# Kernel tuning notes

Hardware: AMD Instinct MI355X
Metric: run time of the kernel (lower is better)

The kernel has to match this reference:

```python
import jax, jax.numpy as jnp
import numpy as np

HEADS, DQK, DV = 4, 128, 128
HH, WW = 32, 32
SCALE = DQK ** -0.5
EPS = 1e-5


def bn(x, g, b, m, v):
    # eval-mode BatchNorm2d over channel dim of NCHW
    inv = g * jax.lax.rsqrt(v + EPS)
    return x * inv[:, None, None] + (b - m * inv)[:, None, None]


def rel_to_abs(x):
    # x: (B, Nh, L, 2L-1) -> (B, Nh, L, L)
    B, Nh, L, _ = x.shape
    x = jnp.pad(x, ((0, 0), (0, 0), (0, 0), (0, 1)))
    fx = x.reshape(B, Nh, L * 2 * L)
    fx = jnp.pad(fx, ((0, 0), (0, 0), (0, L - 1)))
    fx = fx.reshape(B, Nh, L + 1, 2 * L - 1)
    return fx[:, :, :L, L - 1:]


def rel_logits_1d(q, rel_k):
    # q: (B, Nh, H, W, D); rel_k: (2W-1, D)
    B, Nh, H, W, D = q.shape
    r = jnp.einsum('bnhwd,rd->bnhwr', q, rel_k)
    r = rel_to_abs(r.reshape(B, Nh * H, W, 2 * W - 1))
    r = r.reshape(B, Nh, H, W, W)
    return jnp.broadcast_to(r[:, :, :, None], (B, Nh, H, H, W, W))


def pos_bias(q, rel_h, rel_w):
    # q: (B, Nh, H*W, D), already scaled
    B, Nh, L, D = q.shape
    q5 = q.reshape(B, Nh, HH, WW, D)
    rw = rel_logits_1d(q5, rel_w)                     # (B,N,H,Hx,W,W)
    rw = rw.transpose(0, 1, 2, 4, 3, 5).reshape(B, Nh, HH * WW, HH * WW)
    rh = rel_logits_1d(q5.transpose(0, 1, 3, 2, 4), rel_h)  # (B,N,W,Wx,H,H)
    rh = rh.transpose(0, 1, 4, 2, 5, 3).reshape(B, Nh, HH * WW, HH * WW)
    return rw + rh


def to_heads(x):
    # (B, Nh*d, H, W) -> (B, Nh, H*W, d)
    B, C, H, W = x.shape
    x = x.reshape(B, HEADS, C // HEADS, H, W)
    return x.transpose(0, 1, 3, 4, 2).reshape(B, HEADS, H * W, C // HEADS)


def mhsa(x, w_qk, w_v, rel_h, rel_w):
    B, C, H, W = x.shape
    qk = jnp.einsum('bchw,oc->bohw', x, w_qk)
    q, k = jnp.split(qk, 2, axis=1)
    v = jnp.einsum('bchw,oc->bohw', x, w_v)
    q, k, v = to_heads(q), to_heads(k), to_heads(v)
    q = q * SCALE
    logits = jnp.einsum('bnid,bnjd->bnij', q, k) + pos_bias(q, rel_h, rel_w)
    weights = jax.nn.softmax(logits, axis=-1)
    out = jnp.einsum('bnij,bnjd->bnid', weights, v)   # (B,Nh,HW,dv)
    out = out.reshape(B, HEADS, H, W, DV).transpose(0, 1, 4, 2, 3)
    return out.reshape(B, HEADS * DV, H, W)


def setup_inputs() -> dict:
    key = jax.random.key(0)
    ks = jax.random.split(key, 12)
    d = {
        'x': jax.random.normal(ks[0], (8, 512, HH, WW), jnp.float32),
        'w_qk': jax.random.normal(ks[1], (2 * HEADS * DQK, 512), jnp.float32) * 0.02,
        'w_v': jax.random.normal(ks[2], (HEADS * DV, 512), jnp.float32) * 0.02,
        'rel_h': jax.random.normal(ks[3], (2 * HH - 1, DQK), jnp.float32) * SCALE,
        'rel_w': jax.random.normal(ks[4], (2 * WW - 1, DQK), jnp.float32) * SCALE,
        'g1': jnp.ones((512,), jnp.float32),
        'b1': jnp.zeros((512,), jnp.float32),
        'm1': jax.random.normal(ks[5], (512,), jnp.float32) * 0.1,
        'v1': jax.random.uniform(ks[6], (512,), jnp.float32) + 0.5,
        'g2': jnp.ones((512,), jnp.float32),
        'b2': jnp.zeros((512,), jnp.float32),
        'm2': jax.random.normal(ks[7], (512,), jnp.float32) * 0.1,
        'v2': jax.random.uniform(ks[8], (512,), jnp.float32) + 0.5,
        'w_fc': jax.random.normal(ks[9], (512, 512, 3, 3), jnp.float32) * 0.02,
        'bias_fc': jnp.zeros((512,), jnp.float32),
    }
    return d


def reference(x, w_qk, w_v, rel_h, rel_w, g1, b1, m1, v1, g2, b2, m2, v2, w_fc, bias_fc):
    out = jax.nn.relu(bn(x, g1, b1, m1, v1))
    out = mhsa(out, w_qk, w_v, rel_h, rel_w)
    x = out + x
    out = jax.nn.relu(bn(x, g2, b2, m2, v2))
    out = jax.lax.conv_general_dilated(
        out, w_fc, window_strides=(1, 1), padding='SAME',
        dimension_numbers=('NCHW', 'OIHW', 'NCHW')) + bias_fc[:, None, None]
    return out + x
```

## Files before the change

### kernel.cpp

```cpp
#include <hip/hip_runtime.h>

typedef __bf16 v8bf __attribute__((ext_vector_type(8)));
typedef float f32x4 __attribute__((ext_vector_type(4)));

#define DEVI static __device__ __forceinline__

DEVI v8bf load8(const __bf16* p) { return *reinterpret_cast<const v8bf*>(p); }

DEVI f32x4 mfma16(v8bf a, v8bf b, f32x4 c) {
  return __builtin_amdgcn_mfma_f32_16x16x32_bf16(a, b, c, 0, 0, 0);
}

DEVI void gld16(const __bf16* g, __bf16* l) {
  __builtin_amdgcn_global_load_lds(
      (const __attribute__((address_space(1))) unsigned int*)(const void*)g,
      (__attribute__((address_space(3))) unsigned int*)(void*)l, 16, 0, 0);
}

#define SCALE_Q 0.08838834764831845f

__global__ void k_prep(const float* __restrict__ wqk, const float* __restrict__ wv,
                       const float* __restrict__ relh, const float* __restrict__ relw,
                       const float* __restrict__ wfc, __bf16* __restrict__ wqkb,
                       __bf16* __restrict__ wvb, __bf16* __restrict__ rhb,
                       __bf16* __restrict__ rwb, __bf16* __restrict__ Wt,
                       float* __restrict__ zpad4) {
  const int bid = blockIdx.x, tid = threadIdx.x;
  if (bid < 2048) {
    int i = bid * 256 + tid;
    wqkb[i] = (__bf16)wqk[i];
  } else if (bid < 3072) {
    int i = (bid - 2048) * 256 + tid;
    wvb[i] = (__bf16)wv[i];
  } else if (bid < 3104) {
    int i = (bid - 3072) * 256 + tid;
    if (i < 8064) rhb[i] = (__bf16)relh[i];
  } else if (bid < 3136) {
    int i = (bid - 3104) * 256 + tid;
    if (i < 8064) rwb[i] = (__bf16)relw[i];
  } else if (bid < 4160) {
    int i = (bid - 3136) * 256 + tid;
    const float* src = wfc + (size_t)i * 9;
#pragma unroll
    for (int tap = 0; tap < 9; ++tap)
      Wt[(size_t)tap * 262144 + i] = (__bf16)src[tap];
  } else {
    int i = (bid - 4160) * 256 + tid;
    f32x4 z = {0.f, 0.f, 0.f, 0.f};
    reinterpret_cast<f32x4*>(zpad4)[i] = z;
  }
}

__global__ void k_bn1(const float* __restrict__ x, const float* __restrict__ g,
                      const float* __restrict__ bb, const float* __restrict__ m,
                      const float* __restrict__ v, __bf16* __restrict__ y) {
  __shared__ float tile[32][33];
  const int b = blockIdx.z, c0 = blockIdx.y * 32, s0 = blockIdx.x * 32;
  const int tx = threadIdx.x, ty = threadIdx.y;
#pragma unroll
  for (int r = 0; r < 4; ++r) {
    int c = c0 + ty + r * 8;
    float inv = g[c] * rsqrtf(v[c] + 1e-5f);
    float beta = bb[c] - m[c] * inv;
    float val = x[((size_t)b * 512 + c) * 1024 + s0 + tx] * inv + beta;
    tile[ty + r * 8][tx] = fmaxf(val, 0.0f);
  }
  __syncthreads();
#pragma unroll
  for (int r = 0; r < 4; ++r) {
    int s = s0 + ty + r * 8;
    y[((size_t)b * 1024 + s) * 512 + c0 + tx] = (__bf16)tile[tx][ty + r * 8];
  }
}

__global__ void k_bn2(const float* __restrict__ x2, const float* __restrict__ g,
                      const float* __restrict__ bb, const float* __restrict__ m,
                      const float* __restrict__ v, __bf16* __restrict__ zp) {
  __shared__ float tile[32][33];
  const int b = blockIdx.z, c0 = blockIdx.y * 32, s0 = blockIdx.x * 32;
  const int tx = threadIdx.x, ty = threadIdx.y;
#pragma unroll
  for (int r = 0; r < 4; ++r) {
    int c = c0 + ty + r * 8;
    float inv = g[c] * rsqrtf(v[c] + 1e-5f);
    float beta = bb[c] - m[c] * inv;
    float val = x2[((size_t)b * 512 + c) * 1024 + s0 + tx] * inv + beta;
    tile[ty + r * 8][tx] = fmaxf(val, 0.0f);
  }
  __syncthreads();
#pragma unroll
  for (int r = 0; r < 4; ++r) {
    int s = s0 + ty + r * 8;
    int hh = s >> 5, ww = s & 31;
    zp[(((size_t)b * 34 + hh + 1) * 34 + ww + 1) * 512 + c0 + tx] =
        (__bf16)tile[tx][ty + r * 8];
  }
}

__global__ __launch_bounds__(256) void k_proj(
    const __bf16* __restrict__ wall, const __bf16* __restrict__ y,
    __bf16* __restrict__ qout, __bf16* __restrict__ kout,
    __bf16* __restrict__ vout) {
  __shared__ __bf16 As[128 * 32];
  __shared__ __bf16 Bs[128 * 32];
  const int t = threadIdx.x;
  const int wave = t >> 6, lane = t & 63;
  const int l15 = lane & 15, quad = lane >> 4;
  const int mbase = blockIdx.x * 128;
  const int nbase = blockIdx.y * 128;
  const int mh = (wave >> 1) * 64, nh = (wave & 1) * 64;

  const int row0 = t >> 2, part8 = (t & 3) * 8;
  const __bf16* gA0 = wall + (size_t)(mbase + row0) * 512 + part8;
  const __bf16* gA1 = gA0 + (size_t)64 * 512;
  const __bf16* gB0 = y + (size_t)(nbase + row0) * 512 + part8;
  const __bf16* gB1 = gB0 + (size_t)64 * 512;
  __bf16* lA0 = As + (size_t)(wave * 64) * 8;
  __bf16* lA1 = As + (size_t)(256 + wave * 64) * 8;
  __bf16* lB0 = Bs + (size_t)(wave * 64) * 8;
  __bf16* lB1 = Bs + (size_t)(256 + wave * 64) * 8;

  const f32x4 fz = {0.f, 0.f, 0.f, 0.f};
  f32x4 acc[4][4];
#pragma unroll
  for (int i = 0; i < 4; ++i)
#pragma unroll
    for (int j = 0; j < 4; ++j) acc[i][j] = fz;

  for (int k0 = 0; k0 < 512; k0 += 32) {
    __syncthreads();
    gld16(gA0 + k0, lA0);
    gld16(gA1 + k0, lA1);
    gld16(gB0 + k0, lB0);
    gld16(gB1 + k0, lB1);
    __syncthreads();
    v8bf a[4], bfr[4];
#pragma unroll
    for (int i = 0; i < 4; ++i)
      a[i] = load8(&As[(size_t)(mh + i * 16 + l15) * 32 + quad * 8]);
#pragma unroll
    for (int j = 0; j < 4; ++j)
      bfr[j] = load8(&Bs[(size_t)(nh + j * 16 + l15) * 32 + quad * 8]);
#pragma unroll
    for (int i = 0; i < 4; ++i)
#pragma unroll
      for (int j = 0; j < 4; ++j) acc[i][j] = mfma16(a[i], bfr[j], acc[i][j]);
  }

#pragma unroll
  for (int i = 0; i < 4; ++i)
#pragma unroll
    for (int j = 0; j < 4; ++j)
#pragma unroll
      for (int r = 0; r < 4; ++r) {
        int o = mbase + mh + i * 16 + quad * 4 + r;
        int nflat = nbase + nh + j * 16 + l15;
        int b = nflat >> 10, s = nflat & 1023;
        float val = acc[i][j][r];
        if (o < 512) {
          int n = o >> 7, d = o & 127;
          qout[(((size_t)b * 4 + n) * 1024 + s) * 128 + d] = (__bf16)(val * SCALE_Q);
        } else if (o < 1024) {
          int oe = o - 512; int n = oe >> 7, d = oe & 127;
          kout[(((size_t)b * 4 + n) * 1024 + s) * 128 + d] = (__bf16)val;
        } else {
          int oe = o - 1024; int n = oe >> 7, d = oe & 127;
          vout[(((size_t)b * 4 + n) * 128 + d) * 1024 + s] = (__bf16)val;
        }
      }
}

__global__ __launch_bounds__(256, 2) void k_attn(
    const __bf16* __restrict__ q, const __bf16* __restrict__ kmat,
    const __bf16* __restrict__ vt, const __bf16* __restrict__ relh,
    const __bf16* __restrict__ relw, const float* __restrict__ x,
    float* __restrict__ x2) {
  __shared__ __bf16 Ks[4 * 64 * 32];
  __shared__ __bf16 Vs[2 * 128 * 32];
  __shared__ __bf16 P[4 * 16 * 72];
  __shared__ float RWs[64][33];
  __shared__ float RHs[64][33];

  const int Lb = blockIdx.x;
  const int xcd = Lb & 7, local = Lb >> 3;
  const int bn = xcd * 4 + (local & 3);
  const int qblk = local >> 2;
  const int s0 = qblk * 64;

  const int t = threadIdx.x;
  const int wave = t >> 6, lane = t & 63;
  const int l15 = lane & 15, quad = lane >> 4;
  const size_t hoff = ((size_t)bn) << 17;
  const int s0w = s0 + wave * 16;
  const int wlo = (wave & 1) * 16;
  const int h0w = s0w >> 5;

  v8bf aq[4];
  {
    const __bf16* qp = q + hoff + (size_t)(s0w + l15) * 128;
#pragma unroll
    for (int kk = 0; kk < 4; ++kk) aq[kk] = load8(qp + kk * 32 + quad * 8);
  }

#pragma unroll
  for (int nt = 0; nt < 4; ++nt) {
    int rr = nt * 16 + l15;
    const __bf16* bp = relw + (size_t)rr * 128;
    f32x4 acc = {0.f, 0.f, 0.f, 0.f};
#pragma unroll
    for (int kk = 0; kk < 4; ++kk)
      acc = mfma16(aq[kk], load8(bp + kk * 32 + quad * 8), acc);
#pragma unroll
    for (int r = 0; r < 4; ++r) {
      int row = quad * 4 + r;
      int wj = rr + wlo + row - 31;
      if (wj >= 0 && wj < 32) RWs[wave * 16 + row][wj] = acc[r];
    }
  }
#pragma unroll
  for (int nt = 0; nt < 2; ++nt) {
    int hj = nt * 16 + l15;
    const __bf16* bp = relh + (size_t)(hj - h0w + 31) * 128;
    f32x4 acc = {0.f, 0.f, 0.f, 0.f};
#pragma unroll
    for (int kk = 0; kk < 4; ++kk)
      acc = mfma16(aq[kk], load8(bp + kk * 32 + quad * 8), acc);
#pragma unroll
    for (int r = 0; r < 4; ++r) RHs[wave * 16 + quad * 4 + r][hj] = acc[r];
  }

  const int row0 = t >> 2, part8 = (t & 3) * 8;
  const __bf16* kg = kmat + hoff + (size_t)row0 * 128 + part8;
  const __bf16* vg = vt + hoff + (size_t)row0 * 1024 + part8;
  __bf16* ksw = Ks + wave * 512;
  __bf16* vsw = Vs + wave * 512;

  const f32x4 fz = {0.f, 0.f, 0.f, 0.f};
  float lsum[4] = {0.f, 0.f, 0.f, 0.f};
  f32x4 oacc[8];
#pragma unroll
  for (int dt = 0; dt < 8; ++dt) oacc[dt] = fz;
  __bf16* Pw = P + wave * 16 * 72;

#pragma unroll 1
  for (int iter = 0; iter < 16; ++iter) {
    const int j0 = iter * 64;
    __syncthreads();
#pragma unroll
    for (int kk = 0; kk < 4; ++kk)
      gld16(kg + (size_t)j0 * 128 + kk * 32, ksw + kk * 2048);
#pragma unroll
    for (int kk2 = 0; kk2 < 2; ++kk2)
#pragma unroll
      for (int dh = 0; dh < 2; ++dh)
        gld16(vg + (size_t)dh * 64 * 1024 + j0 + kk2 * 32,
              vsw + kk2 * 4096 + dh * 2048);
    __syncthreads();

    f32x4 sacc[4];
#pragma unroll
    for (int nj = 0; nj < 4; ++nj) {
      f32x4 a = fz;
#pragma unroll
      for (int kk = 0; kk < 4; ++kk)
        a = mfma16(aq[kk],
                   load8(&Ks[kk * 2048 + (nj * 16 + l15) * 32 + quad * 8]), a);
      sacc[nj] = a;
    }
#pragma unroll
    for (int nj = 0; nj < 4; ++nj) {
      const int wj = (nj & 1) * 16 + l15;
      const int hj = (j0 + nj * 16) >> 5;
#pragma unroll
      for (int r = 0; r < 4; ++r) {
        const int row = quad * 4 + r;
        const int gi = wave * 16 + row;
        float val = sacc[nj][r] + RWs[gi][wj] + RHs[gi][hj];
        float p = __expf(fminf(val, 60.0f));
        lsum[r] += p;
        Pw[row * 72 + nj * 16 + l15] = (__bf16)p;
      }
    }
    v8bf pf[2];
#pragma unroll
    for (int kk2 = 0; kk2 < 2; ++kk2)
      pf[kk2] = *reinterpret_cast<const v8bf*>(&Pw[l15 * 72 + kk2 * 32 + quad * 8]);
#pragma unroll
    for (int dt = 0; dt < 8; ++dt) {
      f32x4 a = oacc[dt];
#pragma unroll
      for (int kk2 = 0; kk2 < 2; ++kk2)
        a = mfma16(pf[kk2],
                   load8(&Vs[kk2 * 4096 + (dt * 16 + l15) * 32 + quad * 8]), a);
      oacc[dt] = a;
    }
  }

#pragma unroll
  for (int r = 0; r < 4; ++r)
#pragma unroll
    for (int msk = 8; msk >= 1; msk >>= 1) lsum[r] += __shfl_xor(lsum[r], msk);

#pragma unroll
  for (int r = 0; r < 4; ++r) {
    float inv = 1.0f / lsum[r];
    int s = s0w + quad * 4 + r;
#pragma unroll
    for (int dt = 0; dt < 8; ++dt) {
      int d = dt * 16 + l15;
      size_t idx = ((size_t)bn * 128 + d) * 1024 + s;
      x2[idx] = oacc[dt][r] * inv + x[idx];
    }
  }
}

__global__ __launch_bounds__(256, 2) void k_conv(
    const __bf16* __restrict__ Wt, const __bf16* __restrict__ zp,
    float* __restrict__ part) {
  __shared__ __bf16 As[4 * 128 * 32];
  __shared__ __bf16 Bs[4 * 128 * 32];
  const int t = threadIdx.x;
  const int wave = t >> 6, lane = t & 63;
  const int l15 = lane & 15, quad = lane >> 4;

  const int id = blockIdx.x;
  const int combo = id & 7;
  const int ot = combo >> 1, sp = combo & 1;
  const int nt = id >> 3;
  const int mbase = ot * 128;
  const int nbase = nt * 128;
  const int cs = sp * 256;
  const int mh = (wave >> 1) * 64, nh = (wave & 1) * 64;

  const int row0 = t >> 2;
  const int part8 = (t & 3) * 8;
  const __bf16* gA0 = Wt + (size_t)(mbase + row0) * 512 + cs + part8;
  const __bf16* gA1 = gA0 + (size_t)64 * 512;
  const int n0 = nbase + row0;
  const int b0 = n0 >> 10, spn = n0 & 1023;
  const __bf16* gB0 =
      zp + ((size_t)(b0 * 34 + (spn >> 5) + 1) * 34 + (spn & 31) + 1) * 512 + cs + part8;
  const __bf16* gB1 = gB0 + (size_t)2 * 34 * 512;
  const int wofs = wave * 512;

  const f32x4 fz = {0.f, 0.f, 0.f, 0.f};
  f32x4 acc[4][4];
#pragma unroll
  for (int i = 0; i < 4; ++i)
#pragma unroll
    for (int j = 0; j < 4; ++j) acc[i][j] = fz;

#pragma unroll 1
  for (int tap = 0; tap < 9; ++tap) {
    const int dh = tap / 3 - 1, dw = tap % 3 - 1;
    const size_t aoff = (size_t)tap * 512 * 512;
    const int boff = (dh * 34 + dw) * 512;
#pragma unroll 1
    for (int k0 = 0; k0 < 256; k0 += 128) {
      __syncthreads();
#pragma unroll
      for (int c = 0; c < 4; ++c) {
        const int kq = k0 + c * 32;
        gld16(gA0 + aoff + kq, As + c * 4096 + wofs);
        gld16(gA1 + aoff + kq, As + c * 4096 + 2048 + wofs);
        gld16(gB0 + boff + kq, Bs + c * 4096 + wofs);
        gld16(gB1 + boff + kq, Bs + c * 4096 + 2048 + wofs);
      }
      __syncthreads();
#pragma unroll
      for (int c = 0; c < 4; ++c) {
        v8bf a[4], bfr[4];
#pragma unroll
        for (int i = 0; i < 4; ++i)
          a[i] = load8(&As[c * 4096 + (mh + i * 16 + l15) * 32 + quad * 8]);
#pragma unroll
        for (int j = 0; j < 4; ++j)
          bfr[j] = load8(&Bs[c * 4096 + (nh + j * 16 + l15) * 32 + quad * 8]);
#pragma unroll
        for (int i = 0; i < 4; ++i)
#pragma unroll
          for (int j = 0; j < 4; ++j) acc[i][j] = mfma16(a[i], bfr[j], acc[i][j]);
      }
    }
  }

  float* pout = part + (size_t)sp * 8 * 512 * 1024;
#pragma unroll
  for (int i = 0; i < 4; ++i)
#pragma unroll
    for (int j = 0; j < 4; ++j)
#pragma unroll
      for (int r = 0; r < 4; ++r) {
        int o = mbase + mh + i * 16 + quad * 4 + r;
        int nn = nbase + nh + j * 16 + l15;
        int bb2 = nn >> 10, s = nn & 1023;
        pout[((size_t)bb2 * 512 + o) * 1024 + s] = acc[i][j][r];
      }
}

__global__ void k_sum(const float* __restrict__ part, const float* __restrict__ bias,
                      const float* __restrict__ x2, float* __restrict__ out) {
  int i = blockIdx.x * 256 + threadIdx.x;
  int o = (i >> 8) & 511;
  f32x4 p0 = reinterpret_cast<const f32x4*>(part)[i];
  f32x4 p1 = reinterpret_cast<const f32x4*>(part + (size_t)8 * 512 * 1024)[i];
  f32x4 xr = reinterpret_cast<const f32x4*>(x2)[i];
  float bo = bias[o];
  f32x4 r;
#pragma unroll
  for (int c = 0; c < 4; ++c) r[c] = p0[c] + p1[c] + bo + xr[c];
  reinterpret_cast<f32x4*>(out)[i] = r;
}

extern "C" void kernel_launch(void* const* d_in, const int* in_sizes, int n_in,
                              void* d_out, int out_size, void* d_ws, size_t ws_size,
                              hipStream_t stream) {
  const float* x    = (const float*)d_in[0];
  const float* wqk  = (const float*)d_in[1];
  const float* wv   = (const float*)d_in[2];
  const float* relh = (const float*)d_in[3];
  const float* relw = (const float*)d_in[4];
  const float* g1   = (const float*)d_in[5];
  const float* b1   = (const float*)d_in[6];
  const float* m1   = (const float*)d_in[7];
  const float* v1   = (const float*)d_in[8];
  const float* g2   = (const float*)d_in[9];
  const float* b2   = (const float*)d_in[10];
  const float* m2   = (const float*)d_in[11];
  const float* v2   = (const float*)d_in[12];
  const float* wfc  = (const float*)d_in[13];
  const float* bfc  = (const float*)d_in[14];
  float* out = (float*)d_out;

  char* p = (char*)d_ws;
  __bf16* y    = (__bf16*)p; p += (size_t)8 * 1024 * 512 * 2;
  __bf16* qb   = (__bf16*)p; p += (size_t)8 * 4 * 1024 * 128 * 2;
  __bf16* kb   = (__bf16*)p; p += (size_t)8 * 4 * 1024 * 128 * 2;
  __bf16* vb   = (__bf16*)p; p += (size_t)8 * 4 * 1024 * 128 * 2;
  __bf16* Wt   = (__bf16*)p; p += (size_t)9 * 512 * 512 * 2;
  __bf16* wqkb = (__bf16*)p; p += (size_t)1024 * 512 * 2;
  __bf16* wvb  = (__bf16*)p; p += (size_t)512 * 512 * 2;
  __bf16* rhb  = (__bf16*)p; p += 32768;
  __bf16* rwb  = (__bf16*)p; p += 32768;
  float*  x2   = (float*)p;  p += (size_t)8 * 512 * 1024 * 4;
  __bf16* zpad = (__bf16*)p; p += (size_t)8 * 34 * 34 * 512 * 2;
  float* part = (float*)d_ws;

  k_prep<<<dim3(6472), dim3(256), 0, stream>>>(wqk, wv, relh, relw, wfc,
                                               wqkb, wvb, rhb, rwb, Wt, (float*)zpad);
  k_bn1<<<dim3(32, 16, 8), dim3(32, 8), 0, stream>>>(x, g1, b1, m1, v1, y);
  k_proj<<<dim3(12, 64), dim3(256), 0, stream>>>(wqkb, y, qb, kb, vb);
  k_attn<<<dim3(512), dim3(256), 0, stream>>>(qb, kb, vb, rhb, rwb, x, x2);
  k_bn2<<<dim3(32, 16, 8), dim3(32, 8), 0, stream>>>(x2, g2, b2, m2, v2, zpad);
  k_conv<<<dim3(512), dim3(256), 0, stream>>>(Wt, zpad, part);
  k_sum<<<dim3(4096), dim3(256), 0, stream>>>(part, bfc, x2, out);
}
```

Before: 241.6 us.

## Coalesce Q/K projection stores and shrink attention LDS for higher occupancy

In k_proj, the Q and K tiles swap MFMA operand order so each lane holds consecutive head-dim outputs, which is meant to make the per-head row stores coalesced; V keeps the old order for its transposed layout. In k_attn, the relative-position bias tables move from fp32 to bf16 and the P scratch stride drops from 72 to 68. The smaller LDS footprint allows launch bounds of 3 blocks per SM. The bias lookups are hoisted out of the inner nj loop so each row loads its bias values once. The risks are lower bias precision, register pressure under the tighter occupancy target, and a 68-element P stride that leaves the 16-byte vector reads of P not 16-byte aligned.

After: 240.8 us. Within noise of the previous version (-0.4%).

```diff
diff --git a/kernel.cpp b/kernel.cpp
--- a/kernel.cpp
+++ b/kernel.cpp
@@ -109,6 +109,7 @@
   const int mbase = blockIdx.x * 128;
   const int nbase = blockIdx.y * 128;
   const int mh = (wave >> 1) * 64, nh = (wave & 1) * 64;
+  const bool isv = mbase >= 1024;
 
   const int row0 = t >> 2, part8 = (t & 3) * 8;
   const __bf16* gA0 = wall + (size_t)(mbase + row0) * 512 + part8;
@@ -141,45 +142,65 @@
 #pragma unroll
     for (int j = 0; j < 4; ++j)
       bfr[j] = load8(&Bs[(size_t)(nh + j * 16 + l15) * 32 + quad * 8]);
+    if (isv) {
+#pragma unroll
+      for (int i = 0; i < 4; ++i)
+#pragma unroll
+        for (int j = 0; j < 4; ++j) acc[i][j] = mfma16(a[i], bfr[j], acc[i][j]);
+    } else {
+#pragma unroll
+      for (int i = 0; i < 4; ++i)
+#pragma unroll
+        for (int j = 0; j < 4; ++j) acc[i][j] = mfma16(bfr[j], a[i], acc[i][j]);
+    }
+  }
+
+  if (isv) {
 #pragma unroll
     for (int i = 0; i < 4; ++i)
 #pragma unroll
-      for (int j = 0; j < 4; ++j) acc[i][j] = mfma16(a[i], bfr[j], acc[i][j]);
-  }
-
-#pragma unroll
-  for (int i = 0; i < 4; ++i)
-#pragma unroll
-    for (int j = 0; j < 4; ++j)
-#pragma unroll
-      for (int r = 0; r < 4; ++r) {
-        int o = mbase + mh + i * 16 + quad * 4 + r;
-        int nflat = nbase + nh + j * 16 + l15;
-        int b = nflat >> 10, s = nflat & 1023;
-        float val = acc[i][j][r];
-        if (o < 512) {
-          int n = o >> 7, d = o & 127;
-          qout[(((size_t)b * 4 + n) * 1024 + s) * 128 + d] = (__bf16)(val * SCALE_Q);
-        } else if (o < 1024) {
-          int oe = o - 512; int n = oe >> 7, d = oe & 127;
-          kout[(((size_t)b * 4 + n) * 1024 + s) * 128 + d] = (__bf16)val;
-        } else {
+      for (int j = 0; j < 4; ++j)
+#pragma unroll
+        for (int r = 0; r < 4; ++r) {
+          int o = mbase + mh + i * 16 + quad * 4 + r;
+          int nflat = nbase + nh + j * 16 + l15;
+          int b = nflat >> 10, s = nflat & 1023;
           int oe = o - 1024; int n = oe >> 7, d = oe & 127;
-          vout[(((size_t)b * 4 + n) * 128 + d) * 1024 + s] = (__bf16)val;
+          vout[(((size_t)b * 4 + n) * 128 + d) * 1024 + s] = (__bf16)acc[i][j][r];
         }
-      }
-}
-
-__global__ __launch_bounds__(256, 2) void k_attn(
+  } else {
+    const bool isq = mbase < 512;
+#pragma unroll
+    for (int i = 0; i < 4; ++i)
+#pragma unroll
+      for (int j = 0; j < 4; ++j)
+#pragma unroll
+        for (int r = 0; r < 4; ++r) {
+          int o = mbase + mh + i * 16 + l15;
+          int nflat = nbase + nh + j * 16 + quad * 4 + r;
+          int b = nflat >> 10, s = nflat & 1023;
+          float val = acc[i][j][r];
+          if (isq) {
+            int n = o >> 7, d = o & 127;
+            qout[(((size_t)b * 4 + n) * 1024 + s) * 128 + d] = (__bf16)(val * SCALE_Q);
+          } else {
+            int oe = o - 512; int n = oe >> 7, d = oe & 127;
+            kout[(((size_t)b * 4 + n) * 1024 + s) * 128 + d] = (__bf16)val;
+          }
+        }
+  }
+}
+
+__global__ __launch_bounds__(256, 3) void k_attn(
     const __bf16* __restrict__ q, const __bf16* __restrict__ kmat,
     const __bf16* __restrict__ vt, const __bf16* __restrict__ relh,
     const __bf16* __restrict__ relw, const float* __restrict__ x,
     float* __restrict__ x2) {
   __shared__ __bf16 Ks[4 * 64 * 32];
   __shared__ __bf16 Vs[2 * 128 * 32];
-  __shared__ __bf16 P[4 * 16 * 72];
-  __shared__ float RWs[64][33];
-  __shared__ float RHs[64][33];
+  __shared__ __bf16 P[4 * 16 * 68];
+  __shared__ __bf16 RWs[64][33];
+  __shared__ __bf16 RHs[64][33];
 
   const int Lb = blockIdx.x;
   const int xcd = Lb & 7, local = Lb >> 3;
@@ -214,7 +235,7 @@
     for (int r = 0; r < 4; ++r) {
       int row = quad * 4 + r;
       int wj = rr + wlo + row - 31;
-      if (wj >= 0 && wj < 32) RWs[wave * 16 + row][wj] = acc[r];
+      if (wj >= 0 && wj < 32) RWs[wave * 16 + row][wj] = (__bf16)acc[r];
     }
   }
 #pragma unroll
@@ -226,7 +247,7 @@
     for (int kk = 0; kk < 4; ++kk)
       acc = mfma16(aq[kk], load8(bp + kk * 32 + quad * 8), acc);
 #pragma unroll
-    for (int r = 0; r < 4; ++r) RHs[wave * 16 + quad * 4 + r][hj] = acc[r];
+    for (int r = 0; r < 4; ++r) RHs[wave * 16 + quad * 4 + r][hj] = (__bf16)acc[r];
   }
 
   const int row0 = t >> 2, part8 = (t & 3) * 8;
@@ -240,7 +261,7 @@
   f32x4 oacc[8];
 #pragma unroll
   for (int dt = 0; dt < 8; ++dt) oacc[dt] = fz;
-  __bf16* Pw = P + wave * 16 * 72;
+  __bf16* Pw = P + wave * 16 * 68;
 
 #pragma unroll 1
   for (int iter = 0; iter < 16; ++iter) {
@@ -267,24 +288,25 @@
                    load8(&Ks[kk * 2048 + (nj * 16 + l15) * 32 + quad * 8]), a);
       sacc[nj] = a;
     }
-#pragma unroll
-    for (int nj = 0; nj < 4; ++nj) {
-      const int wj = (nj & 1) * 16 + l15;
-      const int hj = (j0 + nj * 16) >> 5;
-#pragma unroll
-      for (int r = 0; r < 4; ++r) {
-        const int row = quad * 4 + r;
-        const int gi = wave * 16 + row;
-        float val = sacc[nj][r] + RWs[gi][wj] + RHs[gi][hj];
+    const int hjb = j0 >> 5;
+#pragma unroll
+    for (int r = 0; r < 4; ++r) {
+      const int row = quad * 4 + r;
+      const int gi = wave * 16 + row;
+      const float rw0 = (float)RWs[gi][l15], rw1 = (float)RWs[gi][l15 + 16];
+      const float rh0 = (float)RHs[gi][hjb], rh1 = (float)RHs[gi][hjb + 1];
+#pragma unroll
+      for (int nj = 0; nj < 4; ++nj) {
+        float val = sacc[nj][r] + ((nj & 1) ? rw1 : rw0) + ((nj & 2) ? rh1 : rh0);
         float p = __expf(fminf(val, 60.0f));
         lsum[r] += p;
-        Pw[row * 72 + nj * 16 + l15] = (__bf16)p;
+        Pw[row * 68 + nj * 16 + l15] = (__bf16)p;
       }
     }
     v8bf pf[2];
 #pragma unroll
     for (int kk2 = 0; kk2 < 2; ++kk2)
-      pf[kk2] = *reinterpret_cast<const v8bf*>(&Pw[l15 * 72 + kk2 * 32 + quad * 8]);
+      pf[kk2] = *reinterpret_cast<const v8bf*>(&Pw[l15 * 68 + kk2 * 32 + quad * 8]);
 #pragma unroll
     for (int dt = 0; dt < 8; ++dt) {
       f32x4 a = oacc[dt];
```
